# Kernel optimization log

Measured on AMD Instinct MI355X. Metric: run time of the kernel, lower is better.

## Reference

```python
import jax, jax.numpy as jnp
import numpy as np

B, N, D, F_IN, E, RATIO, C, HEADS, KERNELS = 128, 512, 128, 128, 524288, 128, 10, 4, 3
ALPHA = 0.5


def setup_inputs() -> dict:
    key = jax.random.key(0)
    ks = jax.random.split(key, 20)

    def w(k, shape, fan):
        return (jax.random.normal(k, shape, jnp.float32) / np.float32(np.sqrt(fan)))

    gid = jnp.arange(E, dtype=jnp.int32) // (E // B)
    src = gid * N + jax.random.randint(ks[0], (E,), 0, N, dtype=jnp.int32)
    dst = gid * N + jax.random.randint(ks[1], (E,), 0, N, dtype=jnp.int32)
    edge_index = jnp.stack([src, dst]).astype(jnp.int32)
    return {
        'x': jax.random.normal(ks[2], (B * N, F_IN), jnp.float32),
        'edge_index': edge_index,
        'enc_w': w(ks[3], (F_IN, D), F_IN), 'enc_b': jnp.zeros((D,), jnp.float32),
        'gconv_w': w(ks[4], (3, KERNELS, D, D), D), 'gconv_b': jnp.zeros((3, KERNELS, D), jnp.float32),
        'wg1_w': w(ks[5], (D,), D), 'wg1_b': jnp.zeros((1,), jnp.float32),
        'wg2_w': w(ks[6], (D,), D), 'wg2_b': jnp.zeros((1,), jnp.float32),
        'pg1_w': w(ks[7], (D,), D), 'pg1_b': jnp.zeros((1,), jnp.float32),
        'pg2_w': w(ks[8], (D,), D), 'pg2_b': jnp.zeros((1,), jnp.float32),
        'q_w': w(ks[9], (D, D), D), 'q_b': jnp.zeros((D,), jnp.float32),
        'k_w': w(ks[10], (D, D), D), 'k_b': jnp.zeros((D,), jnp.float32),
        'v_w': w(ks[11], (D, D), D), 'v_b': jnp.zeros((D,), jnp.float32),
        'o_w': w(ks[12], (D, D), D), 'o_b': jnp.zeros((D,), jnp.float32),
        'ro_w': w(ks[13], (RATIO,), RATIO), 'ro_b': jnp.zeros((1,), jnp.float32),
        'c1_w': w(ks[14], (D, D), D), 'c1_b': jnp.zeros((D,), jnp.float32),
        'c2_w': w(ks[15], (D, C), D), 'c2_b': jnp.zeros((C,), jnp.float32),
    }


def _make_gcn(edge_index, n):
    # PyG GCNConv: add self-loops, symmetric normalization D^-1/2 (A+I) D^-1/2
    src, dst = edge_index[0], edge_index[1]
    deg = jax.ops.segment_sum(jnp.ones(src.shape[0], jnp.float32), dst, num_segments=n) + 1.0
    dinv = jax.lax.rsqrt(deg)
    norm = dinv[src] * dinv[dst]          # [E]
    self_norm = dinv * dinv               # self-loop coefficient

    def gcn(x, W, b):
        h = x @ W                                                  # [n, out]
        out = jax.ops.segment_sum(h[src] * norm[:, None], dst, num_segments=n)
        return out + h * self_norm[:, None] + b
    return gcn


def _forward(x, edge_index, enc_w, enc_b, gconv_w, gconv_b,
             wg1_w, wg1_b, wg2_w, wg2_b, pg1_w, pg1_b, pg2_w, pg2_b,
             q_w, q_b, k_w, k_b, v_w, v_b, o_w, o_b, ro_w, ro_b,
             c1_w, c1_b, c2_w, c2_b):
    n = x.shape[0]
    gcn = _make_gcn(edge_index, n)
    h = x @ enc_w + enc_b                   # node encoder (dropout: eval mode)

    def mkgc(hin, Ws, bs):                  # sum of relu(GCNConv) over kernels
        out = jax.nn.relu(gcn(hin, Ws[0], bs[0]))
        for kk in range(1, Ws.shape[0]):
            out = out + jax.nn.relu(gcn(hin, Ws[kk], bs[kk]))
        return out

    x1 = mkgc(h, gconv_w[0], gconv_b[0])
    x2 = mkgc(x1, gconv_w[1], gconv_b[1])
    x3 = mkgc(x2, gconv_w[2], gconv_b[2])

    def gla_score(xi, w1, b1, w2, b2):      # GLAPool(flag=1): global + local score
        s1 = xi @ w1[:, None] + b1          # [n,1]
        s2 = gcn(xi, w2[:, None], b2)       # [n,1]
        return ALPHA * s1 + (1.0 - ALPHA) * s2

    wts = jnp.concatenate([gla_score(xi, wg1_w, wg1_b, wg2_w, wg2_b)
                           for xi in (x1, x2, x3)], axis=-1)        # [n,3]
    wts = jax.nn.softmax(wts, axis=-1)
    xf = wts[:, 0:1] * x1 + wts[:, 1:2] * x2 + wts[:, 2:3] * x3

    # GLAPool top-k pooling (uniform graph sizes -> dense [B,N])
    score = gla_score(xf, pg1_w, pg1_b, pg2_w, pg2_b)[:, 0].reshape(B, N)
    vals, idx = jax.lax.top_k(score, RATIO)                          # [B,RATIO]
    xd = xf.reshape(B, N, D)
    xp = jnp.take_along_axis(xd, idx[:, :, None], axis=1) * jnp.tanh(vals)[:, :, None]

    # MAB: Q from pooled nodes, K/V = GCNConv over full graph
    dh = D // HEADS
    Qh = (xp @ q_w + q_b).reshape(B, RATIO, HEADS, dh)
    K = gcn(xf, k_w, k_b).reshape(B, N, HEADS, dh)
    V = gcn(xf, v_w, v_b).reshape(B, N, HEADS, dh)
    att = jnp.einsum('bqhd,bkhd->bhqk', Qh, K) / jnp.sqrt(jnp.float32(D))
    A = jax.nn.softmax(att, axis=-1)
    O = Qh + jnp.einsum('bhqk,bkhd->bqhd', A, V)
    O = O.reshape(B, RATIO, D)
    O = O + jax.nn.relu(O @ o_w + o_b)

    # Conv1d(ratio, 1, 1) readout == learned weighted sum over pooled slots
    xg = jnp.einsum('r,brd->bd', ro_w, O) + ro_b                     # [B,D]

    hc = jax.nn.relu(xg @ c1_w + c1_b)
    logp = jax.nn.log_softmax(hc @ c2_w + c2_b, axis=-1)
    return logp, xg


def reference(x, edge_index, enc_w, enc_b, gconv_w, gconv_b,
              wg1_w, wg1_b, wg2_w, wg2_b, pg1_w, pg1_b, pg2_w, pg2_b,
              q_w, q_b, k_w, k_b, v_w, v_b, o_w, o_b, ro_w, ro_b,
              c1_w, c1_b, c2_w, c2_b):
    return _forward(x, edge_index, enc_w, enc_b, gconv_w, gconv_b,
                    wg1_w, wg1_b, wg2_w, wg2_b, pg1_w, pg1_b, pg2_w, pg2_b,
                    q_w, q_b, k_w, k_b, v_w, v_b, o_w, o_b, ro_w, ro_b,
                    c1_w, c1_b, c2_w, c2_b)
```

## Files before the change

### kernel.cpp

```cpp
#include <hip/hip_runtime.h>
#include <math.h>

#define N_NODES 65536
#define NE      524288
#define DD      128
#define BGRAPH  128
#define NPG     512
#define RATIO_K 128
#define NHEAD   4
#define DHEAD   32
#define APSFULL ((size_t)N_NODES * DD)

typedef short bf16x8 __attribute__((ext_vector_type(8)));
typedef float f32x4 __attribute__((ext_vector_type(4)));

union U8 { unsigned short u[8]; bf16x8 v; };

__device__ __forceinline__ unsigned short f2b(float f) {
  unsigned u = __float_as_uint(f);
  unsigned r = u + 0x7fffu + ((u >> 16) & 1u);
  return (unsigned short)(r >> 16);
}
__device__ __forceinline__ float b2f(unsigned short h) {
  return __uint_as_float(((unsigned)h) << 16);
}
__device__ __forceinline__ void split3(float v, unsigned short& h, unsigned short& m, unsigned short& l) {
  h = f2b(v);
  float vm = v - b2f(h);
  m = f2b(vm);
  l = f2b(vm - b2f(m));
}


__global__ void count_kernel(const int* __restrict__ dst, int* __restrict__ cnt) {
  int e = blockIdx.x * 256 + threadIdx.x;
  if (e < NE) atomicAdd(&cnt[dst[e]], 1);
}

__global__ void dinv_kernel(const int* __restrict__ cnt, float* __restrict__ dinv) {
  int i = blockIdx.x * 256 + threadIdx.x;
  if (i < N_NODES) dinv[i] = rsqrtf((float)cnt[i] + 1.0f);
}

__global__ __launch_bounds__(512) void scan_kernel2(const int* __restrict__ cnt, int* __restrict__ rp) {
  __shared__ int part[512];
  int g = blockIdx.x, t = threadIdx.x;
  int v = cnt[g * 512 + t];
  part[t] = v;
  __syncthreads();
  for (int off = 1; off < 512; off <<= 1) {
    int u = (t >= off) ? part[t - off] : 0;
    __syncthreads();
    part[t] += u;
    __syncthreads();
  }
  rp[g * 512 + t] = g * 4096 + part[t] - v;
  if (g == BGRAPH - 1 && t == 511) rp[N_NODES] = NE;
}

__global__ void scatter_kernel(const int* __restrict__ edge, const int* __restrict__ rp,
                               int* __restrict__ fill, const float* __restrict__ dinv,
                               int* __restrict__ col, float* __restrict__ wgt) {
  int e = blockIdx.x * 256 + threadIdx.x;
  if (e >= NE) return;
  int s = edge[e];
  int d = edge[NE + e];
  int p = rp[d] + atomicAdd(&fill[d], 1);
  col[p] = s;
  wgt[p] = dinv[s] * dinv[d];
}

struct WPtrs { const float* p[14]; };

__global__ void wprep_all(WPtrs wp, unsigned short* __restrict__ dstBase) {
  int mat = blockIdx.y;
  int idx = blockIdx.x * 256 + threadIdx.x;
  const float* __restrict__ W = wp.p[mat];
  unsigned short* __restrict__ dst = dstBase + (size_t)mat * 49152;
  int k = idx >> 7, n = idx & 127;
  float v = W[k * 128 + n];
  unsigned short h, m, l;
  split3(v, h, m, l);
  dst[n * 128 + k] = h;
  dst[16384 + n * 128 + k] = m;
  dst[32768 + n * 128 + k] = l;
}

__global__ void split_kernel(const float* __restrict__ src, unsigned short* __restrict__ dst, size_t aps) {
  size_t idx = (size_t)blockIdx.x * 256 + threadIdx.x;
  float4 v = ((const float4*)src)[idx];
  union { unsigned short u[4]; uint2 q; } ph, pm, pl;
  split3(v.x, ph.u[0], pm.u[0], pl.u[0]);
  split3(v.y, ph.u[1], pm.u[1], pl.u[1]);
  split3(v.z, ph.u[2], pm.u[2], pl.u[2]);
  split3(v.w, ph.u[3], pm.u[3], pl.u[3]);
  size_t e = idx * 4;
  *(uint2*)&dst[e] = ph.q;
  *(uint2*)&dst[aps + e] = pm.q;
  *(uint2*)&dst[2 * aps + e] = pl.q;
}

#define WROW 40

template<int NW, bool RELU, bool RES, bool DUAL>
__global__ __launch_bounds__(256, 2) void mfma_gemm3(
    const unsigned short* __restrict__ A3, size_t aps,
    const unsigned short* __restrict__ Wt,
    const float* __restrict__ bias, const float* __restrict__ bias2,
    const float* __restrict__ res,
    float* __restrict__ out, float* __restrict__ out2) {
  __shared__ unsigned short Wlds[NW * 3 * 64 * WROW];
  int tid = threadIdx.x;
  int wave = tid >> 6, lane = tid & 63;
  int c16 = lane & 15, kg = lane >> 4;
  int wrow = (wave >> 1) * 32;
  int wcol = (wave & 1) * 32;
  size_t row0 = (size_t)blockIdx.y * 64 + wrow;
  int n0 = blockIdx.x * 64;

  f32x4 acc[NW][2][2];
  #pragma unroll
  for (int m = 0; m < NW; ++m)
    #pragma unroll
    for (int mi = 0; mi < 2; ++mi)
      #pragma unroll
      for (int ni = 0; ni < 2; ++ni) acc[m][mi][ni] = (f32x4){0.f, 0.f, 0.f, 0.f};

  bf16x8 a[2][3], an[2][3];
  #pragma unroll
  for (int mi = 0; mi < 2; ++mi) {
    size_t ro = (row0 + mi * 16 + c16) * 128 + kg * 8;
    a[mi][0] = *(const bf16x8*)&A3[ro];
    a[mi][1] = *(const bf16x8*)&A3[aps + ro];
    a[mi][2] = *(const bf16x8*)&A3[2 * aps + ro];
  }

  for (int ks = 0; ks < 4; ++ks) {
    if (ks) __syncthreads();
    #pragma unroll
    for (int i = 0; i < NW * 3; ++i) {
      int c = tid + i * 256;
      int u4 = c & 3;
      int n = (c >> 2) & 63;
      int mp = c >> 8;
      *(uint4*)&Wlds[(mp * 64 + n) * WROW + u4 * 8] =
          *(const uint4*)&Wt[(size_t)mp * 16384 + (n0 + n) * 128 + ks * 32 + u4 * 8];
    }
    __syncthreads();

    if (ks < 3) {
      #pragma unroll
      for (int mi = 0; mi < 2; ++mi) {
        size_t ro = (row0 + mi * 16 + c16) * 128 + (ks + 1) * 32 + kg * 8;
        an[mi][0] = *(const bf16x8*)&A3[ro];
        an[mi][1] = *(const bf16x8*)&A3[aps + ro];
        an[mi][2] = *(const bf16x8*)&A3[2 * aps + ro];
      }
    }

    #pragma unroll
    for (int mat = 0; mat < NW; ++mat) {
      #pragma unroll
      for (int ni = 0; ni < 2; ++ni) {
        int nrow = (wcol >> 4) + ni;
        int off = ((mat * 3) * 64 + nrow * 16 + c16) * WROW + kg * 8;
        bf16x8 bh = *(const bf16x8*)&Wlds[off];
        bf16x8 bm = *(const bf16x8*)&Wlds[off + 64 * WROW];
        bf16x8 bl = *(const bf16x8*)&Wlds[off + 128 * WROW];
        #pragma unroll
        for (int mi = 0; mi < 2; ++mi) {
          acc[mat][mi][ni] = __builtin_amdgcn_mfma_f32_16x16x32_bf16(a[mi][0], bh, acc[mat][mi][ni], 0, 0, 0);
          acc[mat][mi][ni] = __builtin_amdgcn_mfma_f32_16x16x32_bf16(a[mi][0], bm, acc[mat][mi][ni], 0, 0, 0);
          acc[mat][mi][ni] = __builtin_amdgcn_mfma_f32_16x16x32_bf16(a[mi][1], bh, acc[mat][mi][ni], 0, 0, 0);
          acc[mat][mi][ni] = __builtin_amdgcn_mfma_f32_16x16x32_bf16(a[mi][0], bl, acc[mat][mi][ni], 0, 0, 0);
          acc[mat][mi][ni] = __builtin_amdgcn_mfma_f32_16x16x32_bf16(a[mi][2], bh, acc[mat][mi][ni], 0, 0, 0);
          acc[mat][mi][ni] = __builtin_amdgcn_mfma_f32_16x16x32_bf16(a[mi][1], bm, acc[mat][mi][ni], 0, 0, 0);
        }
      }
    }

    if (ks < 3) {
      #pragma unroll
      for (int mi = 0; mi < 2; ++mi) {
        a[mi][0] = an[mi][0];
        a[mi][1] = an[mi][1];
        a[mi][2] = an[mi][2];
      }
    }
  }

  #pragma unroll
  for (int mi = 0; mi < 2; ++mi)
    #pragma unroll
    for (int ni = 0; ni < 2; ++ni) {
      int colg = n0 + wcol + ni * 16 + c16;
      #pragma unroll
      for (int r = 0; r < 4; ++r) {
        size_t o = (row0 + mi * 16 + kg * 4 + r) * 128 + colg;
        if (DUAL) {
          out[o]  = acc[0][mi][ni][r] + bias[colg];
          out2[o] = acc[NW - 1][mi][ni][r] + bias2[colg];
        } else if (NW == 3) {
          float g = fmaxf(acc[0][mi][ni][r] + bias[colg], 0.f)
                  + fmaxf(acc[1][mi][ni][r] + bias[128 + colg], 0.f)
                  + fmaxf(acc[2][mi][ni][r] + bias[256 + colg], 0.f);
          out[o] = g;
        } else {
          float g = acc[0][mi][ni][r] + bias[colg];
          if (RELU) g = fmaxf(g, 0.f);
          if (RES) g += res[o];
          out[o] = g;
        }
      }
    }
}

__global__ __launch_bounds__(256) void gemm_k128(
    const float* __restrict__ A, const float* __restrict__ W,
    const float* __restrict__ bias, const float* __restrict__ res,
    float* __restrict__ out, int M, int do_relu) {
  __shared__ float As[8][64];
  __shared__ float Ws[8][128];
  int tid = threadIdx.x;
  int tx = tid & 15;
  int ty = tid >> 4;
  int row0 = blockIdx.x * 64;
  if (row0 >= M) return;
  const float* Ab = A + (size_t)row0 * DD;

  float acc[4][8];
  #pragma unroll
  for (int i = 0; i < 4; ++i)
    #pragma unroll
    for (int j = 0; j < 8; ++j) acc[i][j] = 0.f;

  for (int k0 = 0; k0 < 128; k0 += 8) {
    {
      int e = tid * 2;
      int r = e >> 3, kk = e & 7;
      float2 av = *(const float2*)&Ab[r * DD + k0 + kk];
      As[kk][r] = av.x;
      As[kk + 1][r] = av.y;
    }
    {
      int kk = tid >> 5, c = (tid & 31) * 4;
      float4 wv = *(const float4*)&W[(k0 + kk) * DD + c];
      *(float4*)&Ws[kk][c] = wv;
    }
    __syncthreads();
    #pragma unroll
    for (int kk = 0; kk < 8; ++kk) {
      float4 a4 = *(const float4*)&As[kk][ty * 4];
      float4 b0 = *(const float4*)&Ws[kk][tx * 8];
      float4 b1 = *(const float4*)&Ws[kk][tx * 8 + 4];
      float av[4] = {a4.x, a4.y, a4.z, a4.w};
      float bv[8] = {b0.x, b0.y, b0.z, b0.w, b1.x, b1.y, b1.z, b1.w};
      #pragma unroll
      for (int i = 0; i < 4; ++i)
        #pragma unroll
        for (int j = 0; j < 8; ++j) acc[i][j] += av[i] * bv[j];
    }
    __syncthreads();
  }
  #pragma unroll
  for (int i = 0; i < 4; ++i) {
    int r = row0 + ty * 4 + i;
    size_t base = (size_t)r * DD + tx * 8;
    #pragma unroll
    for (int j = 0; j < 8; ++j) {
      float g = acc[i][j];
      if (bias) g += bias[tx * 8 + j];
      if (do_relu) g = fmaxf(g, 0.f);
      if (res) g += res[base + j];
      out[base + j] = g;
    }
  }
}

__global__ __launch_bounds__(256) void agg4s_kernel(
    const float* __restrict__ H, const int* __restrict__ rp, const int* __restrict__ col,
    const float* __restrict__ wgt, const float* __restrict__ dinv,
    unsigned short* __restrict__ out3) {
  int g = blockIdx.x * 256 + threadIdx.x;
  int node = g >> 5;
  int l = g & 31;
  const float4* H4 = (const float4*)H;
  float dv = dinv[node];
  float4 acc = H4[(size_t)node * 32 + l];
  float sn = dv * dv;
  acc.x *= sn; acc.y *= sn; acc.z *= sn; acc.w *= sn;
  int beg = rp[node], end = rp[node + 1];
  for (int j = beg; j < end; ++j) {
    float w = wgt[j];
    int c = col[j];
    float4 hv = H4[(size_t)c * 32 + l];
    acc.x += w * hv.x; acc.y += w * hv.y; acc.z += w * hv.z; acc.w += w * hv.w;
  }
  union { unsigned short u[4]; uint2 q; } ph, pm, pl;
  split3(acc.x, ph.u[0], pm.u[0], pl.u[0]);
  split3(acc.y, ph.u[1], pm.u[1], pl.u[1]);
  split3(acc.z, ph.u[2], pm.u[2], pl.u[2]);
  split3(acc.w, ph.u[3], pm.u[3], pl.u[3]);
  size_t e = (size_t)node * 128 + l * 4;
  *(uint2*)&out3[e] = ph.q;
  *(uint2*)&out3[APSFULL + e] = pm.q;
  *(uint2*)&out3[2 * APSFULL + e] = pl.q;
}

__global__ __launch_bounds__(256) void dot2_kernel(
    const float* __restrict__ X, const float* __restrict__ w1, const float* __restrict__ w2,
    float* __restrict__ t1, float* __restrict__ t2) {
  int node = (blockIdx.x * 256 + threadIdx.x) >> 6;
  int lane = threadIdx.x & 63;
  if (node >= N_NODES) return;
  const float* xr = X + (size_t)node * DD;
  float a = xr[lane], b = xr[lane + 64];
  float s1 = a * w1[lane] + b * w1[lane + 64];
  float s2 = a * w2[lane] + b * w2[lane + 64];
  #pragma unroll
  for (int off = 32; off > 0; off >>= 1) {
    s1 += __shfl_down(s1, off);
    s2 += __shfl_down(s2, off);
  }
  if (lane == 0) { t1[node] = s1; t2[node] = s2; }
}

__global__ void score_kernel(const float* __restrict__ t1, const float* __restrict__ t2,
                             const int* __restrict__ rp, const int* __restrict__ col,
                             const float* __restrict__ wgt, const float* __restrict__ dinv,
                             const float* __restrict__ b1p, const float* __restrict__ b2p,
                             float* __restrict__ out) {
  int i = blockIdx.x * 256 + threadIdx.x;
  if (i >= N_NODES) return;
  float dv = dinv[i];
  float a2 = dv * dv * t2[i] + b2p[0];
  int beg = rp[i], end = rp[i + 1];
  for (int j = beg; j < end; ++j) a2 += wgt[j] * t2[col[j]];
  out[i] = 0.5f * (t1[i] + b1p[0]) + 0.5f * a2;
}

__global__ void xf_kernel(const float* __restrict__ x1, const float* __restrict__ x2,
                          const float* __restrict__ x3, const float* __restrict__ sc,
                          float* __restrict__ xf) {
  size_t idx = (size_t)blockIdx.x * 256 + threadIdx.x;
  int i = (int)(idx >> 5);
  float s0 = sc[i], s1 = sc[N_NODES + i], s2 = sc[2 * N_NODES + i];
  float mx = fmaxf(s0, fmaxf(s1, s2));
  float e0 = __expf(s0 - mx), e1 = __expf(s1 - mx), e2 = __expf(s2 - mx);
  float inv = 1.f / (e0 + e1 + e2);
  e0 *= inv; e1 *= inv; e2 *= inv;
  float4 a = ((const float4*)x1)[idx];
  float4 b = ((const float4*)x2)[idx];
  float4 c = ((const float4*)x3)[idx];
  float4 o;
  o.x = e0 * a.x + e1 * b.x + e2 * c.x;
  o.y = e0 * a.y + e1 * b.y + e2 * c.y;
  o.z = e0 * a.z + e1 * b.z + e2 * c.z;
  o.w = e0 * a.w + e1 * b.w + e2 * c.w;
  ((float4*)xf)[idx] = o;
}

__global__ __launch_bounds__(512) void topk_kernel(const float* __restrict__ score,
                                                   int* __restrict__ idxO, float* __restrict__ valO) {
  int b = blockIdx.x;
  int t = threadIdx.x;
  __shared__ float s[512];
  float v = score[b * NPG + t];
  s[t] = v;
  __syncthreads();
  int rank = 0;
  for (int j = 0; j < 512; ++j) {
    float u = s[j];
    rank += (u > v) || (u == v && j < t);
  }
  if (rank < RATIO_K) { idxO[b * RATIO_K + rank] = t; valO[b * RATIO_K + rank] = v; }
}

__global__ void xp_kernel(const float* __restrict__ xf, const int* __restrict__ idx,
                          const float* __restrict__ vals, float* __restrict__ xp) {
  size_t e = (size_t)blockIdx.x * 256 + threadIdx.x;
  int b = (int)(e >> 14);
  int r = (int)((e >> 7) & 127);
  int f = (int)(e & 127);
  float tv = tanhf(vals[b * RATIO_K + r]);
  int node = idx[b * RATIO_K + r];
  xp[e] = xf[((size_t)b * NPG + node) * DD + f] * tv;
}

__global__ __launch_bounds__(256) void attn_mfma_kernel(
    const float* __restrict__ Q, const float* __restrict__ K,
    const float* __restrict__ V, float* __restrict__ O) {
  int bb = blockIdx.x >> 2, h = blockIdx.x & 3;
  int tid = threadIdx.x;
  int wave = tid >> 6, lane = tid & 63;
  int c16 = lane & 15, kg = lane >> 4;
  int qbase = wave * 32;
  const float cscale = 0.088388347648318447f;

  __shared__ float Vs[64][34];
  __shared__ unsigned char PwB[4][32 * 144];

  bf16x8 Qh[2], Ql[2];
  #pragma unroll
  for (int qt = 0; qt < 2; ++qt) {
    const float* qp = Q + ((size_t)bb * 128 + qbase + qt * 16 + c16) * 128 + h * 32 + kg * 8;
    float4 f0 = *(const float4*)qp;
    float4 f1 = *(const float4*)(qp + 4);
    float f[8] = {f0.x, f0.y, f0.z, f0.w, f1.x, f1.y, f1.z, f1.w};
    U8 hh, ll;
    #pragma unroll
    for (int j = 0; j < 8; ++j) { hh.u[j] = f2b(f[j]); ll.u[j] = f2b(f[j] - b2f(hh.u[j])); }
    Qh[qt] = hh.v; Ql[qt] = ll.v;
  }

  float m2[2] = {-3.0e38f, -3.0e38f};
  float l2[2] = {0.f, 0.f};
  f32x4 od[2][2];
  #pragma unroll
  for (int dt = 0; dt < 2; ++dt)
    #pragma unroll
    for (int qt = 0; qt < 2; ++qt) od[dt][qt] = (f32x4){0.f, 0.f, 0.f, 0.f};

  for (int kc = 0; kc < NPG; kc += 64) {
    if (kc) __syncthreads();
    {
      int j = tid >> 2, grp = tid & 3;
      const float* vp = V + ((size_t)bb * NPG + kc + j) * 128 + h * 32 + grp * 8;
      float4 v0 = *(const float4*)vp;
      float4 v1 = *(const float4*)(vp + 4);
      float* d = &Vs[j][grp * 8];
      *(float2*)&d[0] = make_float2(v0.x, v0.y);
      *(float2*)&d[2] = make_float2(v0.z, v0.w);
      *(float2*)&d[4] = make_float2(v1.x, v1.y);
      *(float2*)&d[6] = make_float2(v1.z, v1.w);
    }
    __syncthreads();

    f32x4 sac[2][4];
    #pragma unroll
    for (int qt = 0; qt < 2; ++qt)
      #pragma unroll
      for (int kt = 0; kt < 4; ++kt) sac[qt][kt] = (f32x4){0.f, 0.f, 0.f, 0.f};

    #pragma unroll
    for (int kt = 0; kt < 4; ++kt) {
      const float* kp = K + ((size_t)bb * NPG + kc + kt * 16 + c16) * 128 + h * 32 + kg * 8;
      float4 f0 = *(const float4*)kp;
      float4 f1 = *(const float4*)(kp + 4);
      float f[8] = {f0.x, f0.y, f0.z, f0.w, f1.x, f1.y, f1.z, f1.w};
      U8 hh, ll;
      #pragma unroll
      for (int j = 0; j < 8; ++j) { hh.u[j] = f2b(f[j]); ll.u[j] = f2b(f[j] - b2f(hh.u[j])); }
      #pragma unroll
      for (int qt = 0; qt < 2; ++qt) {
        sac[qt][kt] = __builtin_amdgcn_mfma_f32_16x16x32_bf16(hh.v, Qh[qt], sac[qt][kt], 0, 0, 0);
        sac[qt][kt] = __builtin_amdgcn_mfma_f32_16x16x32_bf16(hh.v, Ql[qt], sac[qt][kt], 0, 0, 0);
        sac[qt][kt] = __builtin_amdgcn_mfma_f32_16x16x32_bf16(ll.v, Qh[qt], sac[qt][kt], 0, 0, 0);
      }
    }

    float pj[2][16];
    float scl2[2];
    #pragma unroll
    for (int qt = 0; qt < 2; ++qt) {
      float mc = -3.0e38f;
      #pragma unroll
      for (int kt = 0; kt < 4; ++kt)
        #pragma unroll
        for (int r = 0; r < 4; ++r) {
          float v = sac[qt][kt][r] * cscale;
          pj[qt][kt * 4 + r] = v;
          mc = fmaxf(mc, v);
        }
      mc = fmaxf(mc, __shfl_xor(mc, 16));
      mc = fmaxf(mc, __shfl_xor(mc, 32));
      float mnew = fmaxf(m2[qt], mc);
      float scl = __expf(m2[qt] - mnew);
      float ls = 0.f;
      #pragma unroll
      for (int i = 0; i < 16; ++i) {
        float e = __expf(pj[qt][i] - mnew);
        pj[qt][i] = e;
        ls += e;
      }
      ls += __shfl_xor(ls, 16);
      ls += __shfl_xor(ls, 32);
      l2[qt] = l2[qt] * scl + ls;
      m2[qt] = mnew;
      scl2[qt] = scl;
    }
    #pragma unroll
    for (int dt = 0; dt < 2; ++dt)
      #pragma unroll
      for (int qt = 0; qt < 2; ++qt) {
        #pragma unroll
        for (int r = 0; r < 4; ++r) od[dt][qt][r] *= scl2[qt];
      }

    #pragma unroll
    for (int qt = 0; qt < 2; ++qt) {
      int q32 = qt * 16 + c16;
      unsigned char* pb = &PwB[wave][q32 * 144];
      unsigned sw = (unsigned)((q32 & 7) << 4);
      #pragma unroll
      for (int kt = 0; kt < 4; ++kt)
        #pragma unroll
        for (int rp = 0; rp < 2; ++rp) {
          unsigned pk = (unsigned)f2b(pj[qt][kt * 4 + 2 * rp]) |
                        ((unsigned)f2b(pj[qt][kt * 4 + 2 * rp + 1]) << 16);
          *(unsigned*)&pb[((unsigned)(kt * 32 + kg * 8 + 4 * rp)) ^ sw] = pk;
        }
    }

    #pragma unroll
    for (int kw = 0; kw < 2; ++kw) {
      bf16x8 Pb[2];
      #pragma unroll
      for (int qt = 0; qt < 2; ++qt) {
        int q32 = qt * 16 + c16;
        Pb[qt] = *(const bf16x8*)&PwB[wave][q32 * 144 +
                   (((unsigned)(kw * 64 + kg * 16)) ^ ((unsigned)((q32 & 7) << 4)))];
      }
      #pragma unroll
      for (int dt = 0; dt < 2; ++dt) {
        U8 vh, vl;
        #pragma unroll
        for (int j = 0; j < 8; ++j) {
          float v = Vs[kw * 32 + kg * 8 + j][dt * 16 + c16];
          vh.u[j] = f2b(v);
          vl.u[j] = f2b(v - b2f(vh.u[j]));
        }
        #pragma unroll
        for (int qt = 0; qt < 2; ++qt) {
          od[dt][qt] = __builtin_amdgcn_mfma_f32_16x16x32_bf16(vh.v, Pb[qt], od[dt][qt], 0, 0, 0);
          od[dt][qt] = __builtin_amdgcn_mfma_f32_16x16x32_bf16(vl.v, Pb[qt], od[dt][qt], 0, 0, 0);
        }
      }
    }
  }

  #pragma unroll
  for (int qt = 0; qt < 2; ++qt) {
    float inv = 1.f / l2[qt];
    size_t row = (size_t)bb * 128 + qbase + qt * 16 + c16;
    #pragma unroll
    for (int dt = 0; dt < 2; ++dt)
      #pragma unroll
      for (int r = 0; r < 4; ++r) {
        int colg = h * 32 + dt * 16 + kg * 4 + r;
        O[row * 128 + colg] = Q[row * 128 + colg] + od[dt][qt][r] * inv;
      }
  }
}

__global__ void readout_kernel(const float* __restrict__ O2, const float* __restrict__ ro_w,
                               const float* __restrict__ ro_b, float* __restrict__ xg) {
  int idx = blockIdx.x * 256 + threadIdx.x;
  int b = idx >> 7, d = idx & 127;
  float s = ro_b[0];
  for (int r = 0; r < RATIO_K; ++r) s += ro_w[r] * O2[((size_t)b * RATIO_K + r) * DD + d];
  xg[idx] = s;
}

__global__ __launch_bounds__(64) void head_kernel(const float* __restrict__ hc,
                                                  const float* __restrict__ c2w,
                                                  const float* __restrict__ c2b,
                                                  float* __restrict__ out) {
  int b = blockIdx.x, t = threadIdx.x;
  __shared__ float z[10];
  __shared__ float lse_s;
  if (t < 10) {
    float s = c2b[t];
    for (int k = 0; k < 128; ++k) s += hc[b * 128 + k] * c2w[k * 10 + t];
    z[t] = s;
  }
  __syncthreads();
  if (t == 0) {
    float mx = z[0];
    for (int c = 1; c < 10; ++c) mx = fmaxf(mx, z[c]);
    float sum = 0.f;
    for (int c = 0; c < 10; ++c) sum += expf(z[c] - mx);
    lse_s = mx + logf(sum);
  }
  __syncthreads();
  if (t < 10) out[b * 10 + t] = z[t] - lse_s;
}

extern "C" void kernel_launch(void* const* d_in, const int* in_sizes, int n_in,
                              void* d_out, int out_size, void* d_ws, size_t ws_size,
                              hipStream_t stream) {
  const float* x       = (const float*)d_in[0];
  const int*   edge    = (const int*)d_in[1];
  const float* enc_w   = (const float*)d_in[2];
  const float* enc_b   = (const float*)d_in[3];
  const float* gconv_w = (const float*)d_in[4];
  const float* gconv_b = (const float*)d_in[5];
  const float* wg1_w   = (const float*)d_in[6];
  const float* wg1_b   = (const float*)d_in[7];
  const float* wg2_w   = (const float*)d_in[8];
  const float* wg2_b   = (const float*)d_in[9];
  const float* pg1_w   = (const float*)d_in[10];
  const float* pg1_b   = (const float*)d_in[11];
  const float* pg2_w   = (const float*)d_in[12];
  const float* pg2_b   = (const float*)d_in[13];
  const float* q_w     = (const float*)d_in[14];
  const float* q_b     = (const float*)d_in[15];
  const float* k_w     = (const float*)d_in[16];
  const float* k_b     = (const float*)d_in[17];
  const float* v_w     = (const float*)d_in[18];
  const float* v_b     = (const float*)d_in[19];
  const float* o_w     = (const float*)d_in[20];
  const float* o_b     = (const float*)d_in[21];
  const float* ro_w    = (const float*)d_in[22];
  const float* ro_b    = (const float*)d_in[23];
  const float* c1_w    = (const float*)d_in[24];
  const float* c1_b    = (const float*)d_in[25];
  const float* c2_w    = (const float*)d_in[26];
  const float* c2_b    = (const float*)d_in[27];

  float* outp = (float*)d_out;

  const size_t S = (size_t)N_NODES * DD;
  float* ws    = (float*)d_ws;
  float* slot0 = ws;
  float* slot1 = ws + S;
  float* slot2 = ws + 2 * S;
  float* slot3 = ws + 3 * S;
  float* smallf = ws + 4 * S;
  int*   cnt  = (int*)smallf;
  int*   fill = cnt + N_NODES;
  int*   rp   = fill + N_NODES;
  int*   col  = rp + N_NODES + 8;
  float* wgt  = (float*)(col + NE);
  float* dinv = wgt + NE;
  float* sc   = dinv + N_NODES;
  float* t1   = sc + 3 * N_NODES;
  float* t2   = t1 + N_NODES;
  float* score = t2 + N_NODES;
  int*   tidx = (int*)(score + N_NODES);
  float* tval = (float*)(tidx + BGRAPH * RATIO_K);
  float* hcbuf = tval + BGRAPH * RATIO_K;
  unsigned short* wsW = (unsigned short*)(hcbuf + BGRAPH * DD);
  unsigned short* A3  = wsW + 14 * 49152;

  const size_t SP = (size_t)BGRAPH * RATIO_K * DD;
  float* xp = slot3;
  float* Qm = slot3 + SP;
  float* Om = slot3 + 2 * SP;
  float* O2 = slot3 + 3 * SP;

  hipMemsetAsync(cnt, 0, N_NODES * sizeof(int), stream);
  hipMemsetAsync(fill, 0, N_NODES * sizeof(int), stream);
  count_kernel<<<NE / 256, 256, 0, stream>>>(edge + NE, cnt);
  dinv_kernel<<<N_NODES / 256, 256, 0, stream>>>(cnt, dinv);
  scan_kernel2<<<BGRAPH, 512, 0, stream>>>(cnt, rp);
  scatter_kernel<<<NE / 256, 256, 0, stream>>>(edge, rp, fill, dinv, col, wgt);

  WPtrs wp;
  wp.p[0] = enc_w;
  for (int i = 0; i < 9; ++i) wp.p[1 + i] = gconv_w + (size_t)i * DD * DD;
  wp.p[10] = k_w; wp.p[11] = v_w; wp.p[12] = q_w; wp.p[13] = o_w;
  wprep_all<<<dim3(64, 14), 256, 0, stream>>>(wp, wsW);

  split_kernel<<<(int)(S / 1024), 256, 0, stream>>>(x, A3, S);
  mfma_gemm3<1, false, false, false><<<dim3(2, 1024), 256, 0, stream>>>(
      A3, S, wsW, enc_b, nullptr, nullptr, slot0, nullptr);

  float* lin[4] = {slot0, slot1, slot2, slot3};
  const int AGG_GRID = (N_NODES * 32) / 256;
  for (int l = 0; l < 3; ++l) {
    const float* hin = lin[l];
    float* hout = lin[l + 1];
    agg4s_kernel<<<AGG_GRID, 256, 0, stream>>>(hin, rp, col, wgt, dinv, A3);
    mfma_gemm3<3, true, false, false><<<dim3(2, 1024), 256, 0, stream>>>(
        A3, S, wsW + (size_t)(1 + l * 3) * 49152, gconv_b + (size_t)l * 3 * DD,
        nullptr, nullptr, hout, nullptr);
    dot2_kernel<<<N_NODES / 4, 256, 0, stream>>>(hout, wg1_w, wg2_w, t1, t2);
    score_kernel<<<N_NODES / 256, 256, 0, stream>>>(t1, t2, rp, col, wgt, dinv, wg1_b, wg2_b, sc + (size_t)l * N_NODES);
  }

  float* xf = slot0;
  xf_kernel<<<(N_NODES * 32) / 256, 256, 0, stream>>>(slot1, slot2, slot3, sc, xf);

  dot2_kernel<<<N_NODES / 4, 256, 0, stream>>>(xf, pg1_w, pg2_w, t1, t2);
  score_kernel<<<N_NODES / 256, 256, 0, stream>>>(t1, t2, rp, col, wgt, dinv, pg1_b, pg2_b, score);
  topk_kernel<<<BGRAPH, 512, 0, stream>>>(score, tidx, tval);
  xp_kernel<<<(BGRAPH * RATIO_K * DD) / 256, 256, 0, stream>>>(xf, tidx, tval, xp);

  split_kernel<<<(int)(SP / 1024), 256, 0, stream>>>(xp, A3, SP);
  mfma_gemm3<1, false, false, false><<<dim3(2, 256), 256, 0, stream>>>(
      A3, SP, wsW + 12 * 49152UL, q_b, nullptr, nullptr, Qm, nullptr);

  agg4s_kernel<<<AGG_GRID, 256, 0, stream>>>(xf, rp, col, wgt, dinv, A3);
  mfma_gemm3<2, false, false, true><<<dim3(2, 1024), 256, 0, stream>>>(
      A3, S, wsW + 10 * 49152UL, k_b, v_b, nullptr, slot1, slot2);

  attn_mfma_kernel<<<BGRAPH * NHEAD, 256, 0, stream>>>(Qm, slot1, slot2, Om);

  split_kernel<<<(int)(SP / 1024), 256, 0, stream>>>(Om, A3, SP);
  mfma_gemm3<1, true, true, false><<<dim3(2, 256), 256, 0, stream>>>(
      A3, SP, wsW + 13 * 49152UL, o_b, nullptr, Om, O2, nullptr);

  float* xg = outp + BGRAPH * 10;
  readout_kernel<<<(BGRAPH * DD) / 256, 256, 0, stream>>>(O2, ro_w, ro_b, xg);

  gemm_k128<<<BGRAPH / 64, 256, 0, stream>>>(xg, c1_w, c1_b, nullptr, hcbuf, BGRAPH, 1);
  head_kernel<<<BGRAPH, 64, 0, stream>>>(hcbuf, c2_w, c2_b, outp);
}
```

Measured before the change: 716.8 us.

## Retile split-bf16 MFMA GEMM to 128x32 blocks with full-K weight preload

The 3-way split-bf16 GEMM now uses 128-row by 32-column tiles, with each wave owning 32 full-width rows. The block loads the entire K=128 weight slice for its 32 columns into LDS once, up front, instead of restaging a 32-wide K chunk with barriers on every step. This removes three of the four per-K-step syncthreads and the repeated weight staging, but drops the register prefetch of the next A chunk and uses more LDS per block, which may limit occupancy for the NW=3 variant.

```diff
diff --git a/kernel.cpp b/kernel.cpp
--- a/kernel.cpp
+++ b/kernel.cpp
@@ -100,23 +100,32 @@
   *(uint2*)&dst[2 * aps + e] = pl.q;
 }
 
-#define WROW 40
+#define WROW5 136
 
 template<int NW, bool RELU, bool RES, bool DUAL>
-__global__ __launch_bounds__(256, 2) void mfma_gemm3(
+__global__ __launch_bounds__(256, 2) void mfma_gemm5(
     const unsigned short* __restrict__ A3, size_t aps,
     const unsigned short* __restrict__ Wt,
     const float* __restrict__ bias, const float* __restrict__ bias2,
     const float* __restrict__ res,
     float* __restrict__ out, float* __restrict__ out2) {
-  __shared__ unsigned short Wlds[NW * 3 * 64 * WROW];
+  __shared__ unsigned short Wlds[NW * 3 * 32 * WROW5];
   int tid = threadIdx.x;
   int wave = tid >> 6, lane = tid & 63;
   int c16 = lane & 15, kg = lane >> 4;
-  int wrow = (wave >> 1) * 32;
-  int wcol = (wave & 1) * 32;
-  size_t row0 = (size_t)blockIdx.y * 64 + wrow;
-  int n0 = blockIdx.x * 64;
+  size_t row0 = (size_t)blockIdx.y * 128 + wave * 32;
+  int n0 = blockIdx.x * 32;
+
+  #pragma unroll
+  for (int i = 0; i < NW * 6; ++i) {
+    int c = tid + i * 256;
+    int row = c >> 4;
+    int u = c & 15;
+    int mp = row >> 5, n = row & 31;
+    *(uint4*)&Wlds[row * WROW5 + u * 8] =
+        *(const uint4*)&Wt[(size_t)mp * 16384 + (n0 + n) * 128 + u * 8];
+  }
+  __syncthreads();
 
   f32x4 acc[NW][2][2];
   #pragma unroll
@@ -126,47 +135,26 @@
       #pragma unroll
       for (int ni = 0; ni < 2; ++ni) acc[m][mi][ni] = (f32x4){0.f, 0.f, 0.f, 0.f};
 
-  bf16x8 a[2][3], an[2][3];
-  #pragma unroll
-  for (int mi = 0; mi < 2; ++mi) {
-    size_t ro = (row0 + mi * 16 + c16) * 128 + kg * 8;
-    a[mi][0] = *(const bf16x8*)&A3[ro];
-    a[mi][1] = *(const bf16x8*)&A3[aps + ro];
-    a[mi][2] = *(const bf16x8*)&A3[2 * aps + ro];
-  }
-
+  #pragma unroll
   for (int ks = 0; ks < 4; ++ks) {
-    if (ks) __syncthreads();
-    #pragma unroll
-    for (int i = 0; i < NW * 3; ++i) {
-      int c = tid + i * 256;
-      int u4 = c & 3;
-      int n = (c >> 2) & 63;
-      int mp = c >> 8;
-      *(uint4*)&Wlds[(mp * 64 + n) * WROW + u4 * 8] =
-          *(const uint4*)&Wt[(size_t)mp * 16384 + (n0 + n) * 128 + ks * 32 + u4 * 8];
-    }
-    __syncthreads();
-
-    if (ks < 3) {
-      #pragma unroll
-      for (int mi = 0; mi < 2; ++mi) {
-        size_t ro = (row0 + mi * 16 + c16) * 128 + (ks + 1) * 32 + kg * 8;
-        an[mi][0] = *(const bf16x8*)&A3[ro];
-        an[mi][1] = *(const bf16x8*)&A3[aps + ro];
-        an[mi][2] = *(const bf16x8*)&A3[2 * aps + ro];
-      }
+    bf16x8 a[2][3];
+    #pragma unroll
+    for (int mi = 0; mi < 2; ++mi) {
+      size_t ro = (row0 + mi * 16 + c16) * 128 + ks * 32 + kg * 8;
+      a[mi][0] = *(const bf16x8*)&A3[ro];
+      a[mi][1] = *(const bf16x8*)&A3[aps + ro];
+      a[mi][2] = *(const bf16x8*)&A3[2 * aps + ro];
     }
 
     #pragma unroll
     for (int mat = 0; mat < NW; ++mat) {
       #pragma unroll
       for (int ni = 0; ni < 2; ++ni) {
-        int nrow = (wcol >> 4) + ni;
-        int off = ((mat * 3) * 64 + nrow * 16 + c16) * WROW + kg * 8;
+        int rbase = (mat * 3) * 32 + ni * 16 + c16;
+        int off = rbase * WROW5 + ks * 32 + kg * 8;
         bf16x8 bh = *(const bf16x8*)&Wlds[off];
-        bf16x8 bm = *(const bf16x8*)&Wlds[off + 64 * WROW];
-        bf16x8 bl = *(const bf16x8*)&Wlds[off + 128 * WROW];
+        bf16x8 bm = *(const bf16x8*)&Wlds[off + 32 * WROW5];
+        bf16x8 bl = *(const bf16x8*)&Wlds[off + 64 * WROW5];
         #pragma unroll
         for (int mi = 0; mi < 2; ++mi) {
           acc[mat][mi][ni] = __builtin_amdgcn_mfma_f32_16x16x32_bf16(a[mi][0], bh, acc[mat][mi][ni], 0, 0, 0);
@@ -178,22 +166,13 @@
         }
       }
     }
-
-    if (ks < 3) {
-      #pragma unroll
-      for (int mi = 0; mi < 2; ++mi) {
-        a[mi][0] = an[mi][0];
-        a[mi][1] = an[mi][1];
-        a[mi][2] = an[mi][2];
-      }
-    }
   }
 
   #pragma unroll
   for (int mi = 0; mi < 2; ++mi)
     #pragma unroll
     for (int ni = 0; ni < 2; ++ni) {
-      int colg = n0 + wcol + ni * 16 + c16;
+      int colg = n0 + ni * 16 + c16;
       #pragma unroll
       for (int r = 0; r < 4; ++r) {
         size_t o = (row0 + mi * 16 + kg * 4 + r) * 128 + colg;
@@ -663,7 +642,7 @@
   wprep_all<<<dim3(64, 14), 256, 0, stream>>>(wp, wsW);
 
   split_kernel<<<(int)(S / 1024), 256, 0, stream>>>(x, A3, S);
-  mfma_gemm3<1, false, false, false><<<dim3(2, 1024), 256, 0, stream>>>(
+  mfma_gemm5<1, false, false, false><<<dim3(4, 512), 256, 0, stream>>>(
       A3, S, wsW, enc_b, nullptr, nullptr, slot0, nullptr);
 
   float* lin[4] = {slot0, slot1, slot2, slot3};
@@ -672,7 +651,7 @@
     const float* hin = lin[l];
     float* hout = lin[l + 1];
     agg4s_kernel<<<AGG_GRID, 256, 0, stream>>>(hin, rp, col, wgt, dinv, A3);
-    mfma_gemm3<3, true, false, false><<<dim3(2, 1024), 256, 0, stream>>>(
+    mfma_gemm5<3, true, false, false><<<dim3(4, 512), 256, 0, stream>>>(
         A3, S, wsW + (size_t)(1 + l * 3) * 49152, gconv_b + (size_t)l * 3 * DD,
         nullptr, nullptr, hout, nullptr);
     dot2_kernel<<<N_NODES / 4, 256, 0, stream>>>(hout, wg1_w, wg2_w, t1, t2);
@@ -688,17 +667,17 @@
   xp_kernel<<<(BGRAPH * RATIO_K * DD) / 256, 256, 0, stream>>>(xf, tidx, tval, xp);
 
   split_kernel<<<(int)(SP / 1024), 256, 0, stream>>>(xp, A3, SP);
-  mfma_gemm3<1, false, false, false><<<dim3(2, 256), 256, 0, stream>>>(
+  mfma_gemm5<1, false, false, false><<<dim3(4, 128), 256, 0, stream>>>(
       A3, SP, wsW + 12 * 49152UL, q_b, nullptr, nullptr, Qm, nullptr);
 
   agg4s_kernel<<<AGG_GRID, 256, 0, stream>>>(xf, rp, col, wgt, dinv, A3);
-  mfma_gemm3<2, false, false, true><<<dim3(2, 1024), 256, 0, stream>>>(
+  mfma_gemm5<2, false, false, true><<<dim3(4, 512), 256, 0, stream>>>(
       A3, S, wsW + 10 * 49152UL, k_b, v_b, nullptr, slot1, slot2);
 
   attn_mfma_kernel<<<BGRAPH * NHEAD, 256, 0, stream>>>(Qm, slot1, slot2, Om);
 
   split_kernel<<<(int)(SP / 1024), 256, 0, stream>>>(Om, A3, SP);
-  mfma_gemm3<1, true, true, false><<<dim3(2, 256), 256, 0, stream>>>(
+  mfma_gemm5<1, true, true, false><<<dim3(4, 128), 256, 0, stream>>>(
       A3, SP, wsW + 13 * 49152UL, o_b, nullptr, Om, O2, nullptr);
 
   float* xg = outp + BGRAPH * 10;
```

Measured after the change: 811.5 us. 1.13x slower.
